# Kernel optimization log

Hardware: AMD Instinct MI355X
Metric: run time of the kernel (lower is better)

## Reference

```python
import jax, jax.numpy as jnp
import numpy as np

SEQ, B, I, H = 2048, 64, 256, 256


def setup_inputs() -> dict:
    key = jax.random.key(0)
    ks = jax.random.split(key, 10)
    s_i = 1.0 / np.sqrt(H)
    inp = {
        "X": jax.random.normal(ks[0], (SEQ, B, I), dtype=jnp.float32),
        "D": jax.random.randint(ks[1], (SEQ, B), 0, 2, dtype=jnp.int32),
        "Wih_f": jax.random.uniform(ks[2], (3 * H, I), jnp.float32, -s_i, s_i),
        "Whh_f": jax.random.uniform(ks[3], (3 * H, H), jnp.float32, -s_i, s_i),
        "bih_f": jax.random.uniform(ks[4], (3 * H,), jnp.float32, -s_i, s_i),
        "bhh_f": jax.random.uniform(ks[5], (3 * H,), jnp.float32, -s_i, s_i),
        "Wih_b": jax.random.uniform(ks[6], (3 * H, I), jnp.float32, -s_i, s_i),
        "Whh_b": jax.random.uniform(ks[7], (3 * H, H), jnp.float32, -s_i, s_i),
        "bih_b": jax.random.uniform(ks[8], (3 * H,), jnp.float32, -s_i, s_i),
        "bhh_b": jax.random.uniform(ks[9], (3 * H,), jnp.float32, -s_i, s_i),
    }
    return inp


def _gru_cell(x, h, Wih, Whh, bih, bhh):
    # torch.nn.GRUCell math
    gx = x @ Wih.T + bih  # (B, 3H)
    gh = h @ Whh.T + bhh  # (B, 3H)
    xr, xz, xn = jnp.split(gx, 3, axis=-1)
    hr, hz, hn = jnp.split(gh, 3, axis=-1)
    r = jax.nn.sigmoid(xr + hr)
    z = jax.nn.sigmoid(xz + hz)
    n = jnp.tanh(xn + r * hn)
    return (1.0 - z) * n + z * h


def _masked_scan(X, mask, Wih, Whh, bih, bhh, reverse):
    # mask[t] == 1 -> reset incoming hidden state to zero at step t
    def step(h_prev, xm):
        x_t, m_t = xm
        h_in = (1.0 - m_t)[:, None] * h_prev  # (B, H)
        h_new = _gru_cell(x_t, h_in, Wih, Whh, bih, bhh)
        return h_new, h_new

    h0 = jnp.zeros((X.shape[1], Whh.shape[1]), dtype=X.dtype)
    _, hs = jax.lax.scan(step, h0, (X, mask), reverse=reverse)
    return hs  # (SEQ, B, H)


def reference(X, D, Wih_f, Whh_f, bih_f, bhh_f, Wih_b, Whh_b, bih_b, bhh_b):
    Df = D.astype(X.dtype)
    # forward pass: t>0 uses D[t]; t=0 starts from zeros (carry is zeros anyway)
    h = _masked_scan(X, Df, Wih_f, Whh_f, bih_f, bhh_f, reverse=False)
    # backward pass: step t uses D[t+1]; last step starts from zeros
    Db = jnp.concatenate([Df[1:], jnp.zeros_like(Df[:1])], axis=0)
    hb = _masked_scan(X, Db, Wih_b, Whh_b, bih_b, bhh_b, reverse=True)
    return jnp.concatenate([h, hb], axis=2)  # (SEQ, B, 2H)
```

## Files before the change

kernel.cpp:

```cpp
#include <hip/hip_runtime.h>
#include <cstdint>
#include <cstddef>


#define SEQ 2048
#define BATCH 64

typedef __attribute__((ext_vector_type(8))) short short8;
typedef __attribute__((ext_vector_type(4))) float floatx4;
typedef __attribute__((ext_vector_type(2))) _Float16 h2;

#if defined(__has_builtin)
#if __has_builtin(__builtin_amdgcn_fdot2)
#define HAS_FDOT2 1
#endif
#if __has_builtin(__builtin_amdgcn_update_dpp)
#define HAS_DPP 1
#endif
#endif

__device__ inline float fdot2f(h2 a, h2 b, float c){
#ifdef HAS_FDOT2
  return __builtin_amdgcn_fdot2(a, b, c, false);
#else
  return c + (float)a.x * (float)b.x + (float)a.y * (float)b.y;
#endif
}

__device__ inline float quad_add(float x){
#ifdef HAS_DPP
  int t1 = __builtin_amdgcn_update_dpp(0, __builtin_bit_cast(int, x), 0xB1, 0xF, 0xF, false);
  x += __builtin_bit_cast(float, t1);
  int t2 = __builtin_amdgcn_update_dpp(0, __builtin_bit_cast(int, x), 0x4E, 0xF, 0xF, false);
  x += __builtin_bit_cast(float, t2);
  return x;
#else
  x += __shfl_xor(x, 1);
  x += __shfl_xor(x, 2);
  return x;
#endif
}

__device__ inline unsigned short f2bf(float f){
  union { float f; unsigned int u; } a; a.f = f;
  unsigned int u = a.u;
  unsigned int r = (u + 0x7fffu + ((u >> 16) & 1u)) >> 16;
  return (unsigned short)r;
}

__global__ __launch_bounds__(256) void cvt_x_kernel(const float* __restrict__ X,
                                                    unsigned short* __restrict__ Xb){
  size_t i = (size_t)blockIdx.x * 256 + threadIdx.x;
  float4 v = ((const float4*)X)[i];
  ushort4 o;
  o.x = f2bf(v.x); o.y = f2bf(v.y); o.z = f2bf(v.z); o.w = f2bf(v.w);
  ((ushort4*)Xb)[i] = o;
}

__global__ __launch_bounds__(256) void cvt_w_kernel(const float* __restrict__ Wf,
                                                    const float* __restrict__ Wb,
                                                    unsigned short* __restrict__ Wcat){
  int i = blockIdx.x * 256 + threadIdx.x;
  float v = (i < 768 * 256) ? Wf[i] : Wb[i - 768 * 256];
  Wcat[i] = f2bf(v);
}

__global__ __launch_bounds__(256) void gx_gemm_kernel(
    const unsigned short* __restrict__ Xb,
    const unsigned short* __restrict__ Wcat,
    const float* __restrict__ bih_f, const float* __restrict__ bhh_f,
    const float* __restrict__ bih_b, const float* __restrict__ bhh_b,
    _Float16* __restrict__ GX)
{
  __shared__ unsigned short Al[64][72];
  __shared__ unsigned short Bl[128][72];
  const int tid  = threadIdx.x;
  const int lane = tid & 63;
  const int w    = tid >> 6;
  const size_t m0 = (size_t)blockIdx.x * 64;
  const int    n0 = blockIdx.y * 128;

  floatx4 acc[8];
  #pragma unroll
  for (int i = 0; i < 8; i++) acc[i] = (floatx4)0.f;

  const int ar = tid >> 2, ak = (tid & 3) * 16;
  const int bn = tid >> 1, bk = (tid & 1) * 32;

  for (int kc = 0; kc < 4; kc++){
    const int kb = kc * 64;
    { const uint4* s = (const uint4*)(Xb + (m0 + ar) * 256 + kb + ak);
      uint4 u0 = s[0], u1 = s[1];
      *(uint4*)&Al[ar][ak]     = u0;
      *(uint4*)&Al[ar][ak + 8] = u1;
    }
    { const uint4* s = (const uint4*)(Wcat + (size_t)(n0 + bn) * 256 + kb + bk);
      uint4 u0 = s[0], u1 = s[1], u2 = s[2], u3 = s[3];
      *(uint4*)&Bl[bn][bk]      = u0;
      *(uint4*)&Bl[bn][bk + 8]  = u1;
      *(uint4*)&Bl[bn][bk + 16] = u2;
      *(uint4*)&Bl[bn][bk + 24] = u3;
    }
    __syncthreads();
    #pragma unroll
    for (int ks = 0; ks < 2; ks++){
      const int kl = ks * 32 + (lane >> 4) * 8;
      short8 af = *(const short8*)&Al[w * 16 + (lane & 15)][kl];
      #pragma unroll
      for (int nt = 0; nt < 8; nt++){
        short8 bf = *(const short8*)&Bl[nt * 16 + (lane & 15)][kl];
        acc[nt] = __builtin_amdgcn_mfma_f32_16x16x32_bf16(af, bf, acc[nt], 0, 0, 0);
      }
    }
    __syncthreads();
  }
  #pragma unroll
  for (int nt = 0; nt < 8; nt++){
    const int n_g = n0 + nt * 16 + (lane & 15);
    const int nl  = (n_g < 768) ? n_g : n_g - 768;
    const float* bih = (n_g < 768) ? bih_f : bih_b;
    const float* bhh = (n_g < 768) ? bhh_f : bhh_b;
    const float bias = bih[nl] + ((nl < 512) ? bhh[nl] : 0.f);
    #pragma unroll
    for (int r = 0; r < 4; r++){
      const size_t m_g = m0 + w * 16 + (lane >> 4) * 4 + r;
      GX[m_g * 1536 + n_g] = (_Float16)(acc[nt][r] + bias);
    }
  }
}

#define GH_STRIDE 776
__global__ __launch_bounds__(1024) void gru_scan_kernel(
    const float* __restrict__ Whh_f, const float* __restrict__ Whh_b,
    const float* __restrict__ bhh_f, const float* __restrict__ bhh_b,
    const int* __restrict__ D,
    const _Float16* __restrict__ GX,
    float* __restrict__ out)
{
  const int wg  = blockIdx.x;
  const int dir = wg & 1;
  const int b   = wg >> 1;
  const float* Whh = dir ? Whh_b : Whh_f;
  const float* bhh = dir ? bhh_b : bhh_f;
  const int tid   = threadIdx.x;
  const int j0    = tid >> 3;
  const int kq    = tid & 7;
  const int kbase = kq * 32;

  __shared__ _Float16 hbuf[8 * 40];
  __shared__ float    gh2[2 * GH_STRIDE];

  h2 wreg[6][4][4];
  #pragma unroll
  for (int q = 0; q < 6; q++){
    const float* wr = Whh + (size_t)(j0 + 128 * q) * 256 + kbase;
    #pragma unroll
    for (int c = 0; c < 4; c++){
      float4 f0 = *(const float4*)(wr + c * 8);
      float4 f1 = *(const float4*)(wr + c * 8 + 4);
      wreg[q][c][0] = h2{(_Float16)f0.x, (_Float16)f0.y};
      wreg[q][c][1] = h2{(_Float16)f0.z, (_Float16)f0.w};
      wreg[q][c][2] = h2{(_Float16)f1.x, (_Float16)f1.y};
      wreg[q][c][3] = h2{(_Float16)f1.z, (_Float16)f1.w};
    }
  }

  const bool gate = (tid < 256);
  float h_reg = 0.f;
  float bhhn  = 0.f;
  if (gate){
    bhhn = bhh[512 + tid];
    hbuf[((tid >> 5) * 40) + (tid & 31)] = (_Float16)0.f;
  }
  __syncthreads();

  for (int step = 0; step < SEQ; step++){
    const int t = dir ? (SEQ - 1 - step) : step;

    _Float16 pgr = (_Float16)0.f, pgz = (_Float16)0.f, pgn = (_Float16)0.f;
    int mraw = 0;
    if (gate){
      const _Float16* gx = GX + ((size_t)t * BATCH + b) * 1536 + dir * 768;
      pgr = gx[tid];
      pgz = gx[256 + tid];
      pgn = gx[512 + tid];
      const int tm = dir ? t : ((step < SEQ - 1) ? (t + 1) : t);
      mraw = D[(size_t)tm * BATCH + b];
    }

    float acc[6] = {0.f, 0.f, 0.f, 0.f, 0.f, 0.f};
    #pragma unroll
    for (int c = 0; c < 4; c++){
      uint4 u = *(const uint4*)&hbuf[kq * 40 + c * 8];
      h2 p0 = __builtin_bit_cast(h2, u.x);
      h2 p1 = __builtin_bit_cast(h2, u.y);
      h2 p2 = __builtin_bit_cast(h2, u.z);
      h2 p3 = __builtin_bit_cast(h2, u.w);
      #pragma unroll
      for (int q = 0; q < 6; q++){
        acc[q] = fdot2f(wreg[q][c][0], p0, acc[q]);
        acc[q] = fdot2f(wreg[q][c][1], p1, acc[q]);
        acc[q] = fdot2f(wreg[q][c][2], p2, acc[q]);
        acc[q] = fdot2f(wreg[q][c][3], p3, acc[q]);
      }
    }
    #pragma unroll
    for (int q = 0; q < 6; q++) acc[q] = quad_add(acc[q]);
    if ((tid & 3) == 0){
      float* g = gh2 + ((tid >> 2) & 1) * GH_STRIDE;
      #pragma unroll
      for (int q = 0; q < 6; q++) g[j0 + 128 * q] = acc[q];
    }
    __syncthreads();

    if (gate){
      const int j = tid;
      const float gxr = (float)pgr;
      const float gxz = (float)pgz;
      const float gxn = (float)pgn;
      float mnext = (float)mraw;
      if (dir == 0 && step == SEQ - 1) mnext = 0.f;
      const float ghr = gh2[j]       + gh2[GH_STRIDE + j];
      const float ghz = gh2[256 + j] + gh2[GH_STRIDE + 256 + j];
      const float ghn = gh2[512 + j] + gh2[GH_STRIDE + 512 + j];
      const float r = 1.f / (1.f + __expf(-(gxr + ghr)));
      const float z = 1.f / (1.f + __expf(-(gxz + ghz)));
      const float e = __expf(2.f * (gxn + r * (ghn + bhhn)));
      const float n = 1.f - 2.f / (e + 1.f);
      const float hnew = (1.f - z) * n + z * h_reg;
      const size_t row = (size_t)t * BATCH + b;
      out[row * 512 + dir * 256 + j] = hnew;
      h_reg = (1.f - mnext) * hnew;
      hbuf[((j >> 5) * 40) + (j & 31)] = (_Float16)h_reg;
    }
    __syncthreads();
  }
}

extern "C" void kernel_launch(void* const* d_in, const int* in_sizes, int n_in,
                              void* d_out, int out_size, void* d_ws, size_t ws_size,
                              hipStream_t stream)
{
  const float* X     = (const float*)d_in[0];
  const int*   D     = (const int*)  d_in[1];
  const float* Wih_f = (const float*)d_in[2];
  const float* Whh_f = (const float*)d_in[3];
  const float* bih_f = (const float*)d_in[4];
  const float* bhh_f = (const float*)d_in[5];
  const float* Wih_b = (const float*)d_in[6];
  const float* Whh_b = (const float*)d_in[7];
  const float* bih_b = (const float*)d_in[8];
  const float* bhh_b = (const float*)d_in[9];
  float* out = (float*)d_out;

  char* ws = (char*)d_ws;
  unsigned short* Xb   = (unsigned short*)ws;
  unsigned short* Wcat = (unsigned short*)(ws + 67108864);
  _Float16*       GX   = (_Float16*)(ws + 67895296);

  cvt_x_kernel<<<dim3(32768), 256, 0, stream>>>(X, Xb);
  cvt_w_kernel<<<dim3(1536), 256, 0, stream>>>(Wih_f, Wih_b, Wcat);
  gx_gemm_kernel<<<dim3(2048, 12), 256, 0, stream>>>(Xb, Wcat, bih_f, bhh_f, bih_b, bhh_b, GX);
  gru_scan_kernel<<<dim3(128), 1024, 0, stream>>>(Whh_f, Whh_b, bhh_f, bhh_b, D, GX, out);
}
```

Measured before the change: 3.188 ms.

## Remap Whh rows to threads, reduce over 8 lanes, defer output stores

Each thread group now owns 6 consecutive Whh rows instead of rows strided by 128. The 8-lane k-split is fully reduced with an extra DPP row-shift step, so one lane per group writes all 6 gate partials into a packed shared-memory array with vector stores, and the gate threads read a single value instead of summing two halves. The output store for each step is also postponed to the start of the next step so it overlaps with the GX loads. The costs are an extra cross-lane reduction step and precomputed gather indices with division and modulo by 6.

New measurement: 3.607 ms. 1.13x slower.

```diff
diff --git a/kernel.cpp b/kernel.cpp
--- a/kernel.cpp
+++ b/kernel.cpp
@@ -27,16 +27,19 @@
 #endif
 }
 
-__device__ inline float quad_add(float x){
+__device__ inline float oct_add(float x){
 #ifdef HAS_DPP
   int t1 = __builtin_amdgcn_update_dpp(0, __builtin_bit_cast(int, x), 0xB1, 0xF, 0xF, false);
   x += __builtin_bit_cast(float, t1);
   int t2 = __builtin_amdgcn_update_dpp(0, __builtin_bit_cast(int, x), 0x4E, 0xF, 0xF, false);
   x += __builtin_bit_cast(float, t2);
+  int t3 = __builtin_amdgcn_update_dpp(0, __builtin_bit_cast(int, x), 0x141, 0xF, 0xF, false);
+  x += __builtin_bit_cast(float, t3);
   return x;
 #else
   x += __shfl_xor(x, 1);
   x += __shfl_xor(x, 2);
+  x += __shfl_xor(x, 4);
   return x;
 #endif
 }
@@ -129,7 +132,6 @@
   }
 }
 
-#define GH_STRIDE 776
 __global__ __launch_bounds__(1024) void gru_scan_kernel(
     const float* __restrict__ Whh_f, const float* __restrict__ Whh_b,
     const float* __restrict__ bhh_f, const float* __restrict__ bhh_b,
@@ -148,12 +150,12 @@
   const int kbase = kq * 32;
 
   __shared__ _Float16 hbuf[8 * 40];
-  __shared__ float    gh2[2 * GH_STRIDE];
+  __shared__ float    ghl[128 * 12];
 
   h2 wreg[6][4][4];
   #pragma unroll
   for (int q = 0; q < 6; q++){
-    const float* wr = Whh + (size_t)(j0 + 128 * q) * 256 + kbase;
+    const float* wr = Whh + (size_t)(6 * j0 + q) * 256 + kbase;
     #pragma unroll
     for (int c = 0; c < 4; c++){
       float4 f0 = *(const float4*)(wr + c * 8);
@@ -168,11 +170,18 @@
   const bool gate = (tid < 256);
   float h_reg = 0.f;
   float bhhn  = 0.f;
+  int a_r = 0, a_z = 0, a_n = 0;
   if (gate){
     bhhn = bhh[512 + tid];
     hbuf[((tid >> 5) * 40) + (tid & 31)] = (_Float16)0.f;
+    a_r = (tid / 6) * 12 + (tid % 6);
+    a_z = ((256 + tid) / 6) * 12 + ((256 + tid) % 6);
+    a_n = ((512 + tid) / 6) * 12 + ((512 + tid) % 6);
   }
   __syncthreads();
+
+  float  pend  = 0.f;
+  size_t paddr = 0;
 
   for (int step = 0; step < SEQ; step++){
     const int t = dir ? (SEQ - 1 - step) : step;
@@ -180,6 +189,7 @@
     _Float16 pgr = (_Float16)0.f, pgz = (_Float16)0.f, pgn = (_Float16)0.f;
     int mraw = 0;
     if (gate){
+      if (step > 0) out[paddr] = pend;
       const _Float16* gx = GX + ((size_t)t * BATCH + b) * 1536 + dir * 768;
       pgr = gx[tid];
       pgz = gx[256 + tid];
@@ -205,11 +215,12 @@
       }
     }
     #pragma unroll
-    for (int q = 0; q < 6; q++) acc[q] = quad_add(acc[q]);
-    if ((tid & 3) == 0){
-      float* g = gh2 + ((tid >> 2) & 1) * GH_STRIDE;
-      #pragma unroll
-      for (int q = 0; q < 6; q++) g[j0 + 128 * q] = acc[q];
+    for (int q = 0; q < 6; q++) acc[q] = oct_add(acc[q]);
+    if ((tid & 7) == 0){
+      float4 v0; v0.x = acc[0]; v0.y = acc[1]; v0.z = acc[2]; v0.w = acc[3];
+      float2 v1; v1.x = acc[4]; v1.y = acc[5];
+      *(float4*)&ghl[12 * j0]     = v0;
+      *(float2*)&ghl[12 * j0 + 4] = v1;
     }
     __syncthreads();
 
@@ -220,21 +231,23 @@
       const float gxn = (float)pgn;
       float mnext = (float)mraw;
       if (dir == 0 && step == SEQ - 1) mnext = 0.f;
-      const float ghr = gh2[j]       + gh2[GH_STRIDE + j];
-      const float ghz = gh2[256 + j] + gh2[GH_STRIDE + 256 + j];
-      const float ghn = gh2[512 + j] + gh2[GH_STRIDE + 512 + j];
+      const float ghr = ghl[a_r];
+      const float ghz = ghl[a_z];
+      const float ghn = ghl[a_n];
       const float r = 1.f / (1.f + __expf(-(gxr + ghr)));
       const float z = 1.f / (1.f + __expf(-(gxz + ghz)));
       const float e = __expf(2.f * (gxn + r * (ghn + bhhn)));
       const float n = 1.f - 2.f / (e + 1.f);
       const float hnew = (1.f - z) * n + z * h_reg;
       const size_t row = (size_t)t * BATCH + b;
-      out[row * 512 + dir * 256 + j] = hnew;
+      pend  = hnew;
+      paddr = row * 512 + dir * 256 + j;
       h_reg = (1.f - mnext) * hnew;
       hbuf[((j >> 5) * 40) + (j & 31)] = (_Float16)h_reg;
     }
     __syncthreads();
   }
+  if (gate) out[paddr] = pend;
 }
 
 extern "C" void kernel_launch(void* const* d_in, const int* in_sizes, int n_in,
```

## Remap GRU scan so each 4-thread group owns one hidden unit, single barrier per step

Applied to the files above, without the earlier changes.

Reassigns work in the recurrent scan so each group of 4 lanes computes all three gate dot-products for one hidden unit over 64-wide K slices. After the quad reduction every thread holds the complete gate sums, so the shared gh buffer and the second __syncthreads per step go away, and the hidden state is double-buffered in LDS. This trades the gate-only thread subset for all 1024 threads doing gate math redundantly, and puts longer serial fdot2 chains in each thread.

New measurement: 3.393 ms. +6.4%, slower.

```diff
diff --git a/kernel.cpp b/kernel.cpp
--- a/kernel.cpp
+++ b/kernel.cpp
@@ -129,7 +129,6 @@
   }
 }
 
-#define GH_STRIDE 776
 __global__ __launch_bounds__(1024) void gru_scan_kernel(
     const float* __restrict__ Whh_f, const float* __restrict__ Whh_b,
     const float* __restrict__ bhh_f, const float* __restrict__ bhh_b,
@@ -142,96 +141,79 @@
   const int b   = wg >> 1;
   const float* Whh = dir ? Whh_b : Whh_f;
   const float* bhh = dir ? bhh_b : bhh_f;
-  const int tid   = threadIdx.x;
-  const int j0    = tid >> 3;
-  const int kq    = tid & 7;
-  const int kbase = kq * 32;
-
-  __shared__ _Float16 hbuf[8 * 40];
-  __shared__ float    gh2[2 * GH_STRIDE];
-
-  h2 wreg[6][4][4];
+  const int tid = threadIdx.x;
+  const int j   = tid >> 2;
+  const int kq  = tid & 3;
+
+  __shared__ _Float16 hb[2][4 * 72];
+
+  h2 wreg[3][8][4];
   #pragma unroll
-  for (int q = 0; q < 6; q++){
-    const float* wr = Whh + (size_t)(j0 + 128 * q) * 256 + kbase;
-    #pragma unroll
-    for (int c = 0; c < 4; c++){
+  for (int g = 0; g < 3; g++){
+    const float* wr = Whh + (size_t)(g * 256 + j) * 256 + kq * 64;
+    #pragma unroll
+    for (int c = 0; c < 8; c++){
       float4 f0 = *(const float4*)(wr + c * 8);
       float4 f1 = *(const float4*)(wr + c * 8 + 4);
-      wreg[q][c][0] = h2{(_Float16)f0.x, (_Float16)f0.y};
-      wreg[q][c][1] = h2{(_Float16)f0.z, (_Float16)f0.w};
-      wreg[q][c][2] = h2{(_Float16)f1.x, (_Float16)f1.y};
-      wreg[q][c][3] = h2{(_Float16)f1.z, (_Float16)f1.w};
-    }
-  }
-
-  const bool gate = (tid < 256);
+      wreg[g][c][0] = h2{(_Float16)f0.x, (_Float16)f0.y};
+      wreg[g][c][1] = h2{(_Float16)f0.z, (_Float16)f0.w};
+      wreg[g][c][2] = h2{(_Float16)f1.x, (_Float16)f1.y};
+      wreg[g][c][3] = h2{(_Float16)f1.z, (_Float16)f1.w};
+    }
+  }
+
+  const float bhhn = bhh[512 + j];
   float h_reg = 0.f;
-  float bhhn  = 0.f;
-  if (gate){
-    bhhn = bhh[512 + tid];
-    hbuf[((tid >> 5) * 40) + (tid & 31)] = (_Float16)0.f;
-  }
+  if (tid < 288) hb[0][tid] = (_Float16)0.f;
   __syncthreads();
 
+  const int hw_addr = ((j >> 6) * 72) + (j & 63);
+
   for (int step = 0; step < SEQ; step++){
-    const int t = dir ? (SEQ - 1 - step) : step;
-
-    _Float16 pgr = (_Float16)0.f, pgz = (_Float16)0.f, pgn = (_Float16)0.f;
-    int mraw = 0;
-    if (gate){
-      const _Float16* gx = GX + ((size_t)t * BATCH + b) * 1536 + dir * 768;
-      pgr = gx[tid];
-      pgz = gx[256 + tid];
-      pgn = gx[512 + tid];
-      const int tm = dir ? t : ((step < SEQ - 1) ? (t + 1) : t);
-      mraw = D[(size_t)tm * BATCH + b];
-    }
-
-    float acc[6] = {0.f, 0.f, 0.f, 0.f, 0.f, 0.f};
-    #pragma unroll
-    for (int c = 0; c < 4; c++){
-      uint4 u = *(const uint4*)&hbuf[kq * 40 + c * 8];
+    const int t   = dir ? (SEQ - 1 - step) : step;
+    const int cur = step & 1;
+
+    const _Float16* gx = GX + ((size_t)t * BATCH + b) * 1536 + dir * 768;
+    _Float16 pgr = gx[j];
+    _Float16 pgz = gx[256 + j];
+    _Float16 pgn = gx[512 + j];
+    const int tm = dir ? t : ((step < SEQ - 1) ? (t + 1) : t);
+    const int mraw = D[(size_t)tm * BATCH + b];
+
+    const _Float16* hcur = &hb[cur][kq * 72];
+    float ar = 0.f, az = 0.f, an = 0.f;
+    #pragma unroll
+    for (int c = 0; c < 8; c++){
+      uint4 u = *(const uint4*)&hcur[c * 8];
       h2 p0 = __builtin_bit_cast(h2, u.x);
       h2 p1 = __builtin_bit_cast(h2, u.y);
       h2 p2 = __builtin_bit_cast(h2, u.z);
       h2 p3 = __builtin_bit_cast(h2, u.w);
-      #pragma unroll
-      for (int q = 0; q < 6; q++){
-        acc[q] = fdot2f(wreg[q][c][0], p0, acc[q]);
-        acc[q] = fdot2f(wreg[q][c][1], p1, acc[q]);
-        acc[q] = fdot2f(wreg[q][c][2], p2, acc[q]);
-        acc[q] = fdot2f(wreg[q][c][3], p3, acc[q]);
-      }
-    }
-    #pragma unroll
-    for (int q = 0; q < 6; q++) acc[q] = quad_add(acc[q]);
-    if ((tid & 3) == 0){
-      float* g = gh2 + ((tid >> 2) & 1) * GH_STRIDE;
-      #pragma unroll
-      for (int q = 0; q < 6; q++) g[j0 + 128 * q] = acc[q];
-    }
-    __syncthreads();
-
-    if (gate){
-      const int j = tid;
-      const float gxr = (float)pgr;
-      const float gxz = (float)pgz;
-      const float gxn = (float)pgn;
-      float mnext = (float)mraw;
-      if (dir == 0 && step == SEQ - 1) mnext = 0.f;
-      const float ghr = gh2[j]       + gh2[GH_STRIDE + j];
-      const float ghz = gh2[256 + j] + gh2[GH_STRIDE + 256 + j];
-      const float ghn = gh2[512 + j] + gh2[GH_STRIDE + 512 + j];
-      const float r = 1.f / (1.f + __expf(-(gxr + ghr)));
-      const float z = 1.f / (1.f + __expf(-(gxz + ghz)));
-      const float e = __expf(2.f * (gxn + r * (ghn + bhhn)));
-      const float n = 1.f - 2.f / (e + 1.f);
-      const float hnew = (1.f - z) * n + z * h_reg;
-      const size_t row = (size_t)t * BATCH + b;
-      out[row * 512 + dir * 256 + j] = hnew;
-      h_reg = (1.f - mnext) * hnew;
-      hbuf[((j >> 5) * 40) + (j & 31)] = (_Float16)h_reg;
+      ar = fdot2f(wreg[0][c][0], p0, ar); ar = fdot2f(wreg[0][c][1], p1, ar);
+      ar = fdot2f(wreg[0][c][2], p2, ar); ar = fdot2f(wreg[0][c][3], p3, ar);
+      az = fdot2f(wreg[1][c][0], p0, az); az = fdot2f(wreg[1][c][1], p1, az);
+      az = fdot2f(wreg[1][c][2], p2, az); az = fdot2f(wreg[1][c][3], p3, az);
+      an = fdot2f(wreg[2][c][0], p0, an); an = fdot2f(wreg[2][c][1], p1, an);
+      an = fdot2f(wreg[2][c][2], p2, an); an = fdot2f(wreg[2][c][3], p3, an);
+    }
+    ar = quad_add(ar); az = quad_add(az); an = quad_add(an);
+
+    const float gxr = (float)pgr;
+    const float gxz = (float)pgz;
+    const float gxn = (float)pgn;
+    const float r = 1.f / (1.f + __expf(-(gxr + ar)));
+    const float z = 1.f / (1.f + __expf(-(gxz + az)));
+    const float e = __expf(2.f * (gxn + r * (an + bhhn)));
+    const float n = 1.f - 2.f / (e + 1.f);
+    const float hnew = (1.f - z) * n + z * h_reg;
+
+    float mnext = (float)mraw;
+    if (dir == 0 && step == SEQ - 1) mnext = 0.f;
+    h_reg = (1.f - mnext) * hnew;
+
+    if (kq == 0){
+      out[((size_t)t * BATCH + b) * 512 + dir * 256 + j] = hnew;
+      hb[cur ^ 1][hw_addr] = (_Float16)h_reg;
     }
     __syncthreads();
   }
```
